# Kernel optimization log

Measured on AMD Instinct MI355X. Metric: run time of the kernel, lower is better.

The kernel has to match this reference:

```python
import jax, jax.numpy as jnp
import numpy as np


def make_hadamard(n, seed=1):
    # Sylvester Hadamard matrix with random sign diagonal, orthonormalized.
    assert (n & (n - 1)) == 0, 'n must be a power of 2'
    H = np.array([[1.0]], dtype=np.float32)
    while H.shape[0] < n:
        H = np.block([[H, H], [H, -H]])
    rng = np.random.default_rng(seed)
    signs = rng.choice(np.array([-1.0, 1.0], dtype=np.float32), size=n)
    H = (H * signs[None, :]) / np.sqrt(n, dtype=np.float32)
    return jnp.asarray(H)


def setup_inputs() -> dict:
    key = jax.random.key(0)
    k_x, = jax.random.split(key, 1)
    B, S, D = 4, 4096, 2048
    x = jax.random.normal(k_x, (B, S, D), dtype=jnp.float32)
    scale = jnp.ones((1,), dtype=jnp.float32) * 0.1  # must be > 0
    hadamard = make_hadamard(D)
    return {
        'x': x,
        'scale': scale,
        'hadamard': hadamard,
        'Qn': 8,
        'Qp': 7,
        'num_elements': B * S * D,
    }


def reference(x, scale, hadamard, Qn, Qp, num_elements):
    # grad_scale_mode == 'LSQ_grad_scale'
    qn = float(Qn)
    qp = float(Qp)
    grad_scale = 1.0 / jnp.sqrt(jnp.float32(num_elements) * qp)
    # scale = (scale - scale*gs).detach() + scale*gs  (forward value unchanged)
    bw_scale = scale * grad_scale
    s = jax.lax.stop_gradient(scale - bw_scale) + bw_scale  # shape [1]

    x_rot = jnp.matmul(x, hadamard)           # [B,S,D]
    xq = jnp.clip(x_rot / s, -qn, qp)
    # straight-through rounding: (round(x)-x).detach() + x
    yq = jax.lax.stop_gradient(jnp.round(xq) - xq) + xq
    y = yq * s
    return jnp.matmul(y, hadamard.T)          # un-rotate
```

## Files before the change

### kernel.cpp

```cpp
#include <hip/hip_runtime.h>
#include <math.h>


constexpr int D  = 2048;
constexpr int NR = 8;

#define LGKM0() __asm__ __volatile__("s_waitcnt lgkmcnt(0)" ::: "memory")

__device__ __forceinline__ void bfly(float4& a, float4& b) {
    float4 ta = a, tb = b;
    a.x = ta.x + tb.x; a.y = ta.y + tb.y; a.z = ta.z + tb.z; a.w = ta.w + tb.w;
    b.x = ta.x - tb.x; b.y = ta.y - tb.y; b.z = ta.z - tb.z; b.w = ta.w - tb.w;
}

__device__ __forceinline__ void reg_stages(float4 (&v)[NR]) {
    #pragma unroll
    for (int m = 1; m <= 4; m <<= 1) {
        #pragma unroll
        for (int r = 0; r < NR; ++r)
            if ((r & m) == 0) bfly(v[r], v[r | m]);
    }
}

__device__ __forceinline__ void comp_stages(float4 (&v)[NR]) {
    #pragma unroll
    for (int r = 0; r < NR; ++r) {
        float a, b;
        a = v[r].x; b = v[r].y; v[r].x = a + b; v[r].y = a - b;
        a = v[r].z; b = v[r].w; v[r].z = a + b; v[r].w = a - b;
        a = v[r].x; b = v[r].z; v[r].x = a + b; v[r].z = a - b;
        a = v[r].y; b = v[r].w; v[r].y = a + b; v[r].w = a - b;
    }
}

__device__ __forceinline__ float quant1(float xh, float h0, float s, float inv_s,
                                        float nqn, float qp) {
    float u = xh * h0 * inv_s;
    u = fminf(fmaxf(u, nqn), qp);
    float q = rintf(u);
    return q * (s * h0);
}

__global__ __launch_bounds__(256) void lsq_fwht_kernel(
    const float* __restrict__ x,
    const float* __restrict__ scale,
    const float* __restrict__ hadamard,
    const int*   __restrict__ qn_p,
    const int*   __restrict__ qp_p,
    const int*   __restrict__ ne_p,
    float*       __restrict__ out,
    int rows)
{
    __shared__ float smem[4][D];

    const int lane = threadIdx.x & 63;
    const int wave = threadIdx.x >> 6;
    const int row  = blockIdx.x * 4 + wave;
    if (row >= rows) return;

    float* lds = smem[wave];
    const int llo = lane & 7;
    const int lhi = lane >> 3;

    const float sc    = scale[0];
    const float qp    = (float)qp_p[0];
    const float nqn   = -(float)qn_p[0];
    const float gs    = 1.0f / sqrtf((float)ne_p[0] * qp);
    const float bw    = sc * gs;
    const float s     = (sc - bw) + bw;
    const float inv_s = 1.0f / s;

    float4 v[NR];
    {
        const float4* x4 = reinterpret_cast<const float4*>(x + (size_t)row * D) + lane;
        #pragma unroll
        for (int r = 0; r < NR; ++r) v[r] = x4[(size_t)r * 64];
    }
    float4 h[NR];
    {
        const float4* h4 = reinterpret_cast<const float4*>(hadamard);
        #pragma unroll
        for (int r = 0; r < NR; ++r) h[r] = h4[lhi * 64 + r * 8 + llo];
    }

    const int wA  = (lane * 4) ^ (lhi << 2);
    const int rBb = lhi * 256 + llo * 32;
    const int rCb = lhi * 256 + ((llo * 4) ^ (lhi << 2));

    comp_stages(v);
    reg_stages(v);
    #pragma unroll
    for (int r = 0; r < NR; ++r)
        *reinterpret_cast<float4*>(lds + r * 256 + wA) = v[r];
    LGKM0();
    #pragma unroll
    for (int r = 0; r < NR; ++r)
        v[r] = *reinterpret_cast<const float4*>(lds + rBb + ((r * 4) ^ (llo << 2)));
    reg_stages(v);
    #pragma unroll
    for (int r = 0; r < NR; ++r)
        *reinterpret_cast<float4*>(lds + rBb + ((r * 4) ^ (lhi << 2))) = v[r];
    LGKM0();
    #pragma unroll
    for (int r = 0; r < NR; ++r)
        v[r] = *reinterpret_cast<const float4*>(lds + rCb + r * 32);
    reg_stages(v);

    #pragma unroll
    for (int r = 0; r < NR; ++r) {
        v[r].x = quant1(v[r].x, h[r].x, s, inv_s, nqn, qp);
        v[r].y = quant1(v[r].y, h[r].y, s, inv_s, nqn, qp);
        v[r].z = quant1(v[r].z, h[r].z, s, inv_s, nqn, qp);
        v[r].w = quant1(v[r].w, h[r].w, s, inv_s, nqn, qp);
    }

    reg_stages(v);
    #pragma unroll
    for (int r = 0; r < NR; ++r)
        *reinterpret_cast<float4*>(lds + rCb + r * 32) = v[r];
    LGKM0();
    #pragma unroll
    for (int r = 0; r < NR; ++r)
        v[r] = *reinterpret_cast<const float4*>(lds + rBb + ((r * 4) ^ (lhi << 2)));
    reg_stages(v);
    #pragma unroll
    for (int r = 0; r < NR; ++r)
        *reinterpret_cast<float4*>(lds + rBb + ((r * 4) ^ (llo << 2))) = v[r];
    LGKM0();
    #pragma unroll
    for (int r = 0; r < NR; ++r)
        v[r] = *reinterpret_cast<const float4*>(lds + r * 256 + wA);
    reg_stages(v);
    comp_stages(v);

    {
        float4* y4 = reinterpret_cast<float4*>(out + (size_t)row * D) + lane;
        #pragma unroll
        for (int r = 0; r < NR; ++r) y4[(size_t)r * 64] = v[r];
    }
}

extern "C" void kernel_launch(void* const* d_in, const int* in_sizes, int n_in,
                              void* d_out, int out_size, void* d_ws, size_t ws_size,
                              hipStream_t stream) {
    const float* x        = (const float*)d_in[0];
    const float* scale    = (const float*)d_in[1];
    const float* hadamard = (const float*)d_in[2];
    const int*   Qn       = (const int*)d_in[3];
    const int*   Qp       = (const int*)d_in[4];
    const int*   ne       = (const int*)d_in[5];
    float*       out      = (float*)d_out;

    const int rows = in_sizes[0] / D;
    const int grid = (rows + 3) / 4;

    lsq_fwht_kernel<<<grid, 256, 0, stream>>>(x, scale, hadamard, Qn, Qp, ne,
                                              out, rows);
}
```

Baseline: 247.6 us.

## Replace one LDS transpose round per direction with cross-lane permlane swap butterflies

Two FWHT butterfly stages per transform now run across lanes using v_permlane16/32_swap instead of a second LDS write/read transpose. This cuts the LDS round trips from two to one per direction, and the LDS layout and hadamard-sign gather are reindexed to match. A runtime probe at kernel start picks which swap semantics variant applies, falling back to shfl_xor. The cost is extra permlane and VALU instructions plus the probe work on every wave.

```diff
diff --git a/kernel.cpp b/kernel.cpp
--- a/kernel.cpp
+++ b/kernel.cpp
@@ -6,6 +6,8 @@
 constexpr int NR = 8;
 
 #define LGKM0() __asm__ __volatile__("s_waitcnt lgkmcnt(0)" ::: "memory")
+
+typedef unsigned uint2v __attribute__((ext_vector_type(2)));
 
 __device__ __forceinline__ void bfly(float4& a, float4& b) {
     float4 ta = a, tb = b;
@@ -30,6 +32,91 @@
         a = v[r].z; b = v[r].w; v[r].z = a + b; v[r].w = a - b;
         a = v[r].x; b = v[r].z; v[r].x = a + b; v[r].z = a - b;
         a = v[r].y; b = v[r].w; v[r].y = a + b; v[r].w = a - b;
+    }
+}
+
+__device__ __forceinline__ void plswap32(float& x, float& y) {
+#if __has_builtin(__builtin_amdgcn_permlane32_swap)
+    uint2v t = __builtin_amdgcn_permlane32_swap(
+        __builtin_bit_cast(unsigned, x), __builtin_bit_cast(unsigned, y),
+        false, false);
+    x = __builtin_bit_cast(float, t[0]);
+    y = __builtin_bit_cast(float, t[1]);
+#else
+    asm volatile("v_permlane32_swap_b32 %0, %1" : "+v"(x), "+v"(y));
+#endif
+}
+__device__ __forceinline__ void plswap16(float& x, float& y) {
+#if __has_builtin(__builtin_amdgcn_permlane16_swap)
+    uint2v t = __builtin_amdgcn_permlane16_swap(
+        __builtin_bit_cast(unsigned, x), __builtin_bit_cast(unsigned, y),
+        false, false);
+    x = __builtin_bit_cast(float, t[0]);
+    y = __builtin_bit_cast(float, t[1]);
+#else
+    asm volatile("v_permlane16_swap_b32 %0, %1" : "+v"(x), "+v"(y));
+#endif
+}
+
+template<bool IS32>
+__device__ __forceinline__ int probe_var(int lane) {
+    const int m = IS32 ? 32 : 16;
+    float a = (float)lane, b = 1000.0f + (float)lane;
+    if (IS32) plswap32(a, b); else plswap16(a, b);
+    const bool hi = (lane & m) != 0;
+    const float ea0 = hi ? 1000.0f + (float)(lane - m) : (float)lane;
+    const float eb0 = hi ? 1000.0f + (float)lane       : (float)(lane + m);
+    const float ea2 = hi ? (float)lane                 : 1000.0f + (float)(lane + m);
+    const float eb2 = hi ? (float)(lane - m)           : 1000.0f + (float)lane;
+    if (__all(a == ea0 && b == eb0)) return 0;
+    if (__all(a == eb0 && b == ea0)) return 1;
+    if (__all(a == ea2 && b == eb2)) return 2;
+    if (__all(a == eb2 && b == ea2)) return 3;
+    return 4;
+}
+
+template<int VAR, bool IS32>
+__device__ __forceinline__ void bfly_l(float& a, float& b) {
+    if (IS32) plswap32(a, b); else plswap16(a, b);
+    float s = a + b;
+    float d = (VAR == 0 || VAR == 3) ? (a - b) : (b - a);
+    if (VAR == 0)      { if (IS32) plswap32(s, d); else plswap16(s, d); a = s; b = d; }
+    else if (VAR == 1) { if (IS32) plswap32(s, d); else plswap16(s, d); a = d; b = s; }
+    else if (VAR == 2) { if (IS32) plswap32(d, s); else plswap16(d, s); a = d; b = s; }
+    else               { if (IS32) plswap32(d, s); else plswap16(d, s); a = s; b = d; }
+}
+
+template<int VAR, bool IS32>
+__device__ __forceinline__ void perm_stage_t(float4 (&v)[NR]) {
+    #pragma unroll
+    for (int r = 0; r < NR; r += 2) {
+        bfly_l<VAR, IS32>(v[r].x, v[r + 1].x);
+        bfly_l<VAR, IS32>(v[r].y, v[r + 1].y);
+        bfly_l<VAR, IS32>(v[r].z, v[r + 1].z);
+        bfly_l<VAR, IS32>(v[r].w, v[r + 1].w);
+    }
+}
+
+__device__ __forceinline__ void shfl_stage(float4 (&v)[NR], int m, int lane) {
+    const bool hi = (lane & m) != 0;
+    #pragma unroll
+    for (int r = 0; r < NR; ++r) {
+        float t;
+        t = __shfl_xor(v[r].x, m); v[r].x = hi ? t - v[r].x : v[r].x + t;
+        t = __shfl_xor(v[r].y, m); v[r].y = hi ? t - v[r].y : v[r].y + t;
+        t = __shfl_xor(v[r].z, m); v[r].z = hi ? t - v[r].z : v[r].z + t;
+        t = __shfl_xor(v[r].w, m); v[r].w = hi ? t - v[r].w : v[r].w + t;
+    }
+}
+
+template<bool IS32>
+__device__ __forceinline__ void perm_stage(float4 (&v)[NR], int var, int lane) {
+    switch (var) {
+    case 0: perm_stage_t<0, IS32>(v); break;
+    case 1: perm_stage_t<1, IS32>(v); break;
+    case 2: perm_stage_t<2, IS32>(v); break;
+    case 3: perm_stage_t<3, IS32>(v); break;
+    default: shfl_stage(v, IS32 ? 32 : 16, lane); break;
     }
 }
 
@@ -59,8 +146,9 @@
     if (row >= rows) return;
 
     float* lds = smem[wave];
-    const int llo = lane & 7;
-    const int lhi = lane >> 3;
+
+    const int v32 = probe_var<true>(lane);
+    const int v16 = probe_var<false>(lane);
 
     const float sc    = scale[0];
     const float qp    = (float)qp_p[0];
@@ -76,35 +164,33 @@
         #pragma unroll
         for (int r = 0; r < NR; ++r) v[r] = x4[(size_t)r * 64];
     }
+
+    const int rB0 = (((lane >> 5) & 1) << 5) + ((lane & 31) << 6);
+
     float4 h[NR];
     {
-        const float4* h4 = reinterpret_cast<const float4*>(hadamard);
-        #pragma unroll
-        for (int r = 0; r < NR; ++r) h[r] = h4[lhi * 64 + r * 8 + llo];
-    }
-
-    const int wA  = (lane * 4) ^ (lhi << 2);
-    const int rBb = lhi * 256 + llo * 32;
-    const int rCb = lhi * 256 + ((llo * 4) ^ (lhi << 2));
+        const float* hp = hadamard + rB0;
+        #pragma unroll
+        for (int q = 0; q < NR; ++q)
+            h[q] = *reinterpret_cast<const float4*>(hp + (q << 2));
+    }
+
+    const int wA0 = (lane << 2) ^ (((lane >> 4) & 3) << 2);
+    const int l7s = (lane & 7) << 2;
 
     comp_stages(v);
     reg_stages(v);
+    perm_stage<false>(v, v16, lane);
+    perm_stage<true >(v, v32, lane);
     #pragma unroll
     for (int r = 0; r < NR; ++r)
-        *reinterpret_cast<float4*>(lds + r * 256 + wA) = v[r];
+        *reinterpret_cast<float4*>(lds + (r << 8) + (wA0 ^ ((r & 1) << 4))) = v[r];
     LGKM0();
     #pragma unroll
-    for (int r = 0; r < NR; ++r)
-        v[r] = *reinterpret_cast<const float4*>(lds + rBb + ((r * 4) ^ (llo << 2)));
-    reg_stages(v);
-    #pragma unroll
-    for (int r = 0; r < NR; ++r)
-        *reinterpret_cast<float4*>(lds + rBb + ((r * 4) ^ (lhi << 2))) = v[r];
-    LGKM0();
-    #pragma unroll
-    for (int r = 0; r < NR; ++r)
-        v[r] = *reinterpret_cast<const float4*>(lds + rCb + r * 32);
-    reg_stages(v);
+    for (int q = 0; q < NR; ++q)
+        v[q] = *reinterpret_cast<const float4*>(lds + rB0 + ((q << 2) ^ l7s));
+    reg_stages(v);
+    perm_stage<true >(v, v32, lane);
 
     #pragma unroll
     for (int r = 0; r < NR; ++r) {
@@ -115,22 +201,17 @@
     }
 
     reg_stages(v);
+    perm_stage<true >(v, v32, lane);
+    #pragma unroll
+    for (int q = 0; q < NR; ++q)
+        *reinterpret_cast<float4*>(lds + rB0 + ((q << 2) ^ l7s)) = v[q];
+    LGKM0();
     #pragma unroll
     for (int r = 0; r < NR; ++r)
-        *reinterpret_cast<float4*>(lds + rCb + r * 32) = v[r];
-    LGKM0();
-    #pragma unroll
-    for (int r = 0; r < NR; ++r)
-        v[r] = *reinterpret_cast<const float4*>(lds + rBb + ((r * 4) ^ (lhi << 2)));
-    reg_stages(v);
-    #pragma unroll
-    for (int r = 0; r < NR; ++r)
-        *reinterpret_cast<float4*>(lds + rBb + ((r * 4) ^ (llo << 2))) = v[r];
-    LGKM0();
-    #pragma unroll
-    for (int r = 0; r < NR; ++r)
-        v[r] = *reinterpret_cast<const float4*>(lds + r * 256 + wA);
-    reg_stages(v);
+        v[r] = *reinterpret_cast<const float4*>(lds + (r << 8) + (wA0 ^ ((r & 1) << 4)));
+    reg_stages(v);
+    perm_stage<false>(v, v16, lane);
+    perm_stage<true >(v, v32, lane);
     comp_stages(v);
 
     {
```

Measured after the change: 245.6 us. About the same (-0.8%).
